# Performance work log

Measured on AMD Instinct MI355X. Metric: run time of the kernel, lower is better.

Reference implementation:

```python
import jax, jax.numpy as jnp
import numpy as np

MASS, CHARGE, ALPHA, BETA = 1.0, 0.5, 0.1, 0.05
ETA = jnp.array([1.0, -1.0, -1.0, -1.0], dtype=jnp.float32)  # Minkowski metric diag


def setup_inputs() -> dict:
    key = jax.random.key(0)
    k1, k2, k3 = jax.random.split(key, 3)
    B = 262144
    y = jax.random.normal(k1, (B, 8), dtype=jnp.float32)
    W = jax.random.normal(k2, (4, 4), dtype=jnp.float32) * 0.3
    V = jax.random.normal(k3, (4, 4), dtype=jnp.float32) * 0.3
    return {"y": y, "W": W, "V": V}


def _lagrangian(z):
    # z = (x, u, A) concatenated, shape [12]
    x, u, A = z[0:4], z[4:8], z[8:12]
    kinetic = 0.5 * MASS * jnp.sum(ETA * u * u)
    coupling = CHARGE * jnp.sum(ETA * u * A)
    xu_term = ALPHA * jnp.sum((x * u) ** 2)      # makes J_xu nontrivial
    uA_term = BETA * jnp.sum(u * A) ** 2          # makes J_Au nontrivial
    return kinetic + coupling + xu_term + uA_term


def reference(y, W, V):
    def A_vec(x):  # vector potential A^mu(x), works on [4] or [B,4]
        return jnp.tanh(x @ W.T) + x @ V.T

    x = y[:, 0:4]   # [B,4] positions
    u = y[:, 4:8]   # [B,4] velocities
    A = A_vec(x)    # [B,4]
    z = jnp.concatenate([x, u, A], axis=1)  # [B,12] = (x,u,A)

    gradL = jax.vmap(jax.grad(_lagrangian))(z)      # [B,12]
    H = jax.vmap(jax.hessian(_lagrangian))(z)       # [B,12,12]

    dL_dx = gradL[:, 0:4]
    dL_dA = gradL[:, 8:12]
    J_xu = H[:, 0:4, 4:8]    # d^2L/(dx^mu du^nu)
    J_uu = H[:, 4:8, 4:8]    # d^2L/(du^mu du^nu)
    J_Au = H[:, 8:12, 4:8]   # d^2L/(dA^mu du^nu)

    # dA_dx[a, nu, i] = dA^i/dx^nu (matches tf.stack(..., axis=2) layout)
    jacA = jax.vmap(jax.jacfwd(A_vec))(x)           # [B, i, nu]
    dA_dx = jnp.transpose(jacA, (0, 2, 1))          # [B, nu, i]

    J_uu_inv = jnp.linalg.pinv(J_uu)                # [B,4,4]

    force = (dL_dx
             + jnp.einsum('ajk,ak->aj', dA_dx, dL_dA)
             - jnp.einsum('ai,aij->aj', u,
                          J_xu + jnp.einsum('ajk,akm->ajm', dA_dx, J_Au)))
    acceleration = jnp.einsum('ai,aij->aj', force, J_uu_inv)  # [B,4]
    return acceleration
```

## Files before the change

kernel.cpp:

```cpp
#include <hip/hip_runtime.h>
#include <math.h>


__global__ __launch_bounds__(256) void rel_particle_kernel(
    const float* __restrict__ y, const float* __restrict__ W,
    const float* __restrict__ V, float* __restrict__ out, int B)
{
    __shared__ double sW[16], sV[16];
    if (threadIdx.x < 16)      sW[threadIdx.x]      = (double)W[threadIdx.x];
    else if (threadIdx.x < 32) sV[threadIdx.x - 16] = (double)V[threadIdx.x - 16];
    __syncthreads();

    int i = blockIdx.x * blockDim.x + threadIdx.x;
    if (i >= B) return;

    const float4* y4 = (const float4*)y;
    float4 xv = y4[2 * i];
    float4 uv = y4[2 * i + 1];
    double x[4] = {xv.x, xv.y, xv.z, xv.w};
    double u[4] = {uv.x, uv.y, uv.z, uv.w};
    const double eta[4] = {1.0, -1.0, -1.0, -1.0};
    const double CHG = 0.5, ALPHA = 0.1, BETA = 0.05;
    const double C2 = 2.0 * BETA;

    double A[4], G[4][4];
    #pragma unroll
    for (int j = 0; j < 4; ++j) {
        double t = 0.0, s = 0.0;
        #pragma unroll
        for (int k = 0; k < 4; ++k) {
            t += sW[j * 4 + k] * x[k];
            s += sV[j * 4 + k] * x[k];
        }
        double th = tanh(t);
        A[j] = th + s;
        double dth = 1.0 - th * th;
        #pragma unroll
        for (int k = 0; k < 4; ++k)
            G[j][k] = dth * sW[j * 4 + k] + sV[j * 4 + k];
    }

    double S = 0.0;
    #pragma unroll
    for (int k = 0; k < 4; ++k) S += u[k] * A[k];

    double P[4], R[4], Q[4];
    #pragma unroll
    for (int j = 0; j < 4; ++j) {
        double p = 0.0, r = 0.0, q = 0.0;
        #pragma unroll
        for (int k = 0; k < 4; ++k) {
            p += G[k][j] * u[k];
            r += G[j][k] * u[k];
            q += G[k][j] * (CHG * eta[k]) * u[k];
        }
        P[j] = p; R[j] = r; Q[j] = q;
    }
    double T = 0.0;
    #pragma unroll
    for (int j = 0; j < 4; ++j) T += u[j] * R[j];

    double f[4];
    #pragma unroll
    for (int j = 0; j < 4; ++j) {
        f[j] = -2.0 * ALPHA * x[j] * u[j] * u[j]
             + Q[j]
             + 2.0 * BETA * S * P[j]
             - (CHG * eta[j] + 2.0 * BETA * S) * R[j]
             - 2.0 * BETA * A[j] * T;
    }

    double d[4], mind = 1e300;
    #pragma unroll
    for (int j = 0; j < 4; ++j) {
        d[j] = eta[j] + 2.0 * ALPHA * x[j] * x[j];
        double a = fabs(d[j]);
        mind = (a < mind) ? a : mind;
    }

    double p01 = d[0] * d[1], p23 = d[2] * d[3];
    double det = p01 * p23;
    {
        double padj0 = d[1] * p23, padj1 = d[0] * p23;
        double padj2 = p01 * d[3], padj3 = p01 * d[2];
        det += C2 * (A[0]*A[0]*padj0 + A[1]*A[1]*padj1 +
                     A[2]*A[2]*padj2 + A[3]*A[3]*padj3);
    }

    double sumA2 = 0.0, sumA4 = 0.0, F2 = 0.0;
    #pragma unroll
    for (int j = 0; j < 4; ++j) {
        double Aj2 = A[j] * A[j];
        sumA2 += Aj2; sumA4 += Aj2 * Aj2;
        double Jjj = d[j] + C2 * Aj2;
        F2 += Jjj * Jjj;
    }
    F2 += C2 * C2 * (sumA2 * sumA2 - sumA4);
    double rowmax = 0.0;
    #pragma unroll
    for (int r = 0; r < 4; ++r) {
        double rs = 0.0;
        #pragma unroll
        for (int c = 0; c < 4; ++c) {
            double Jrc = C2 * A[r] * A[c] + ((r == c) ? d[r] : 0.0);
            rs += fabs(Jrc);
        }
        rowmax = (rs > rowmax) ? rs : rowmax;
    }
    double sig_hi2 = rowmax * rowmax;
    sig_hi2 = (F2 < sig_hi2) ? F2 : sig_hi2;
    bool safe = (fabs(det) > 2.8610229e-5 * sig_hi2 * sig_hi2) && (mind > 1e-3);

    double acc[4];
    if (safe) {
        double b[4], fd[4], den = 1.0, w = 0.0;
        #pragma unroll
        for (int j = 0; j < 4; ++j) {
            double inv = 1.0 / d[j];
            b[j]  = A[j] * inv;
            fd[j] = f[j] * inv;
            den  += C2 * A[j] * b[j];
            w    += b[j] * f[j];
        }
        double scale = C2 * w / den;
        #pragma unroll
        for (int j = 0; j < 4; ++j) acc[j] = fd[j] - b[j] * scale;
    } else {
        double M[4][4], Vm[4][4];
        #pragma unroll
        for (int r = 0; r < 4; ++r) {
            #pragma unroll
            for (int c2i = 0; c2i < 4; ++c2i) {
                M[r][c2i] = C2 * A[r] * A[c2i];
                Vm[r][c2i] = (r == c2i) ? 1.0 : 0.0;
            }
            M[r][r] += d[r];
        }
        for (int sweep = 0; sweep < 8; ++sweep) {
            #pragma unroll
            for (int p = 0; p < 3; ++p) {
                #pragma unroll
                for (int q2 = p + 1; q2 < 4; ++q2) {
                    double apq = M[p][q2];
                    if (fabs(apq) < 1e-280) continue;
                    double app = M[p][p], aqq = M[q2][q2];
                    double tau = (aqq - app) / (2.0 * apq);
                    double tt = ((tau >= 0.0) ? 1.0 : -1.0) /
                                (fabs(tau) + sqrt(1.0 + tau * tau));
                    double c = 1.0 / sqrt(1.0 + tt * tt);
                    double s = tt * c;
                    #pragma unroll
                    for (int k = 0; k < 4; ++k) {
                        double mkp = M[k][p], mkq = M[k][q2];
                        M[k][p]  = c * mkp - s * mkq;
                        M[k][q2] = s * mkp + c * mkq;
                    }
                    #pragma unroll
                    for (int k = 0; k < 4; ++k) {
                        double mpk = M[p][k], mqk = M[q2][k];
                        M[p][k]  = c * mpk - s * mqk;
                        M[q2][k] = s * mpk + c * mqk;
                    }
                    #pragma unroll
                    for (int k = 0; k < 4; ++k) {
                        double vkp = Vm[k][p], vkq = Vm[k][q2];
                        Vm[k][p]  = c * vkp - s * vkq;
                        Vm[k][q2] = s * vkp + c * vkq;
                    }
                }
            }
        }
        double lam[4], sigmax = 0.0;
        #pragma unroll
        for (int k = 0; k < 4; ++k) {
            lam[k] = M[k][k];
            double a = fabs(lam[k]);
            sigmax = (a > sigmax) ? a : sigmax;
        }
        double cutoff = 4.76837158203125e-6 * sigmax;
        #pragma unroll
        for (int j = 0; j < 4; ++j) acc[j] = 0.0;
        #pragma unroll
        for (int e = 0; e < 4; ++e) {
            if (fabs(lam[e]) > cutoff) {
                double coef = 0.0;
                #pragma unroll
                for (int k = 0; k < 4; ++k) coef += Vm[k][e] * f[k];
                coef /= lam[e];
                #pragma unroll
                for (int j = 0; j < 4; ++j) acc[j] += coef * Vm[j][e];
            }
        }
    }

    float4 res;
    res.x = (float)acc[0];
    res.y = (float)acc[1];
    res.z = (float)acc[2];
    res.w = (float)acc[3];
    ((float4*)out)[i] = res;
}

extern "C" void kernel_launch(void* const* d_in, const int* in_sizes, int n_in,
                              void* d_out, int out_size, void* d_ws, size_t ws_size,
                              hipStream_t stream) {
    const float* y = (const float*)d_in[0];
    const float* W = (const float*)d_in[1];
    const float* V = (const float*)d_in[2];
    float* out = (float*)d_out;
    int B = in_sizes[0] / 8;
    int block = 256;
    int grid = (B + block - 1) / block;
    rel_particle_kernel<<<grid, block, 0, stream>>>(y, W, V, out, B);
}
```

Before: 98.32 us.

## Split ill-conditioned particles into a compacted second pass for Jacobi solve

The fast kernel now handles only well-conditioned particles with the Sherman-Morrison solve. Particles that need the pseudo-inverse are appended to a workspace list through an atomic counter. A second small kernel recomputes the model terms for those listed particles and runs the Jacobi eigen-solve, which keeps the heavy branch out of the main kernel's register pressure and warp divergence. The cost is a memset, an extra launch, atomics, and recomputation for the flagged elements. If the workspace overflows, the remaining particles fall back to the Sherman-Morrison solve, which can be inaccurate.

```diff
diff --git a/kernel.cpp b/kernel.cpp
--- a/kernel.cpp
+++ b/kernel.cpp
@@ -2,9 +2,151 @@
 #include <math.h>
 
 
-__global__ __launch_bounds__(256) void rel_particle_kernel(
+#define SIX_RCOND 2.86102294921875e-5
+#define RCOND     4.76837158203125e-6
+
+__device__ __forceinline__ void model_terms(
+    const double* sW, const double* sV,
+    const double x[4], const double u[4],
+    double A[4], double f[4], double d[4])
+{
+    const double eta[4] = {1.0, -1.0, -1.0, -1.0};
+    const double CHG = 0.5, ALPHA = 0.1, BETA = 0.05;
+    double G[4][4];
+    #pragma unroll
+    for (int j = 0; j < 4; ++j) {
+        double t = 0.0, s = 0.0;
+        #pragma unroll
+        for (int k = 0; k < 4; ++k) { t += sW[j*4+k]*x[k]; s += sV[j*4+k]*x[k]; }
+        double th = tanh(t);
+        A[j] = th + s;
+        double dth = 1.0 - th * th;
+        #pragma unroll
+        for (int k = 0; k < 4; ++k) G[j][k] = dth * sW[j*4+k] + sV[j*4+k];
+    }
+    double S = 0.0;
+    #pragma unroll
+    for (int k = 0; k < 4; ++k) S += u[k] * A[k];
+    double P[4], R[4], Q[4];
+    #pragma unroll
+    for (int j = 0; j < 4; ++j) {
+        double p = 0.0, r = 0.0, q = 0.0;
+        #pragma unroll
+        for (int k = 0; k < 4; ++k) {
+            p += G[k][j] * u[k];
+            r += G[j][k] * u[k];
+            q += G[k][j] * (CHG * eta[k]) * u[k];
+        }
+        P[j] = p; R[j] = r; Q[j] = q;
+    }
+    double T = 0.0;
+    #pragma unroll
+    for (int j = 0; j < 4; ++j) T += u[j] * R[j];
+    #pragma unroll
+    for (int j = 0; j < 4; ++j) {
+        f[j] = -2.0 * ALPHA * x[j] * u[j] * u[j]
+             + Q[j]
+             + 2.0 * BETA * S * P[j]
+             - (CHG * eta[j] + 2.0 * BETA * S) * R[j]
+             - 2.0 * BETA * A[j] * T;
+        d[j] = eta[j] + 2.0 * ALPHA * x[j] * x[j];
+    }
+}
+
+__device__ __forceinline__ void sm_solve(
+    const double d[4], const double A[4], const double f[4], double acc[4])
+{
+    const double C2 = 0.1;
+    double b[4], fd[4], den = 1.0, w = 0.0;
+    #pragma unroll
+    for (int j = 0; j < 4; ++j) {
+        double inv = 1.0 / d[j];
+        b[j]  = A[j] * inv;
+        fd[j] = f[j] * inv;
+        den  += C2 * A[j] * b[j];
+        w    += b[j] * f[j];
+    }
+    double scale = C2 * w / den;
+    #pragma unroll
+    for (int j = 0; j < 4; ++j) acc[j] = fd[j] - b[j] * scale;
+}
+
+__device__ void jacobi_pinv_solve(
+    const double d[4], const double A[4], const double f[4], double acc[4])
+{
+    const double C2 = 0.1;
+    double M[4][4], Vm[4][4];
+    #pragma unroll
+    for (int r = 0; r < 4; ++r) {
+        #pragma unroll
+        for (int c = 0; c < 4; ++c) {
+            M[r][c] = C2 * A[r] * A[c];
+            Vm[r][c] = (r == c) ? 1.0 : 0.0;
+        }
+        M[r][r] += d[r];
+    }
+    for (int sweep = 0; sweep < 8; ++sweep) {
+        #pragma unroll
+        for (int p = 0; p < 3; ++p) {
+            #pragma unroll
+            for (int q2 = p + 1; q2 < 4; ++q2) {
+                double apq = M[p][q2];
+                if (fabs(apq) < 1e-280) continue;
+                double app = M[p][p], aqq = M[q2][q2];
+                double tau = (aqq - app) / (2.0 * apq);
+                double tt = ((tau >= 0.0) ? 1.0 : -1.0) /
+                            (fabs(tau) + sqrt(1.0 + tau * tau));
+                double c = 1.0 / sqrt(1.0 + tt * tt);
+                double s = tt * c;
+                #pragma unroll
+                for (int k = 0; k < 4; ++k) {
+                    double mkp = M[k][p], mkq = M[k][q2];
+                    M[k][p]  = c * mkp - s * mkq;
+                    M[k][q2] = s * mkp + c * mkq;
+                }
+                #pragma unroll
+                for (int k = 0; k < 4; ++k) {
+                    double mpk = M[p][k], mqk = M[q2][k];
+                    M[p][k]  = c * mpk - s * mqk;
+                    M[q2][k] = s * mpk + c * mqk;
+                }
+                #pragma unroll
+                for (int k = 0; k < 4; ++k) {
+                    double vkp = Vm[k][p], vkq = Vm[k][q2];
+                    Vm[k][p]  = c * vkp - s * vkq;
+                    Vm[k][q2] = s * vkp + c * vkq;
+                }
+            }
+        }
+    }
+    double lam[4], sigmax = 0.0;
+    #pragma unroll
+    for (int k = 0; k < 4; ++k) {
+        lam[k] = M[k][k];
+        double a = fabs(lam[k]);
+        sigmax = (a > sigmax) ? a : sigmax;
+    }
+    double cutoff = RCOND * sigmax;
+    #pragma unroll
+    for (int j = 0; j < 4; ++j) acc[j] = 0.0;
+    #pragma unroll
+    for (int e = 0; e < 4; ++e) {
+        if (fabs(lam[e]) > cutoff) {
+            double coef = 0.0;
+            #pragma unroll
+            for (int k = 0; k < 4; ++k) coef += Vm[k][e] * f[k];
+            coef /= lam[e];
+            #pragma unroll
+            for (int j = 0; j < 4; ++j) acc[j] += coef * Vm[j][e];
+        }
+    }
+}
+
+__global__ __launch_bounds__(256) void fast_kernel(
     const float* __restrict__ y, const float* __restrict__ W,
-    const float* __restrict__ V, float* __restrict__ out, int B)
+    const float* __restrict__ V, float* __restrict__ out,
+    unsigned int* __restrict__ cnt, int* __restrict__ list,
+    unsigned int cap, int B)
 {
     __shared__ double sW[16], sV[16];
     if (threadIdx.x < 16)      sW[threadIdx.x]      = (double)W[threadIdx.x];
@@ -19,74 +161,21 @@
     float4 uv = y4[2 * i + 1];
     double x[4] = {xv.x, xv.y, xv.z, xv.w};
     double u[4] = {uv.x, uv.y, uv.z, uv.w};
-    const double eta[4] = {1.0, -1.0, -1.0, -1.0};
-    const double CHG = 0.5, ALPHA = 0.1, BETA = 0.05;
-    const double C2 = 2.0 * BETA;
-
-    double A[4], G[4][4];
-    #pragma unroll
-    for (int j = 0; j < 4; ++j) {
-        double t = 0.0, s = 0.0;
-        #pragma unroll
-        for (int k = 0; k < 4; ++k) {
-            t += sW[j * 4 + k] * x[k];
-            s += sV[j * 4 + k] * x[k];
-        }
-        double th = tanh(t);
-        A[j] = th + s;
-        double dth = 1.0 - th * th;
-        #pragma unroll
-        for (int k = 0; k < 4; ++k)
-            G[j][k] = dth * sW[j * 4 + k] + sV[j * 4 + k];
-    }
-
-    double S = 0.0;
-    #pragma unroll
-    for (int k = 0; k < 4; ++k) S += u[k] * A[k];
-
-    double P[4], R[4], Q[4];
-    #pragma unroll
-    for (int j = 0; j < 4; ++j) {
-        double p = 0.0, r = 0.0, q = 0.0;
-        #pragma unroll
-        for (int k = 0; k < 4; ++k) {
-            p += G[k][j] * u[k];
-            r += G[j][k] * u[k];
-            q += G[k][j] * (CHG * eta[k]) * u[k];
-        }
-        P[j] = p; R[j] = r; Q[j] = q;
-    }
-    double T = 0.0;
-    #pragma unroll
-    for (int j = 0; j < 4; ++j) T += u[j] * R[j];
-
-    double f[4];
-    #pragma unroll
-    for (int j = 0; j < 4; ++j) {
-        f[j] = -2.0 * ALPHA * x[j] * u[j] * u[j]
-             + Q[j]
-             + 2.0 * BETA * S * P[j]
-             - (CHG * eta[j] + 2.0 * BETA * S) * R[j]
-             - 2.0 * BETA * A[j] * T;
-    }
-
-    double d[4], mind = 1e300;
-    #pragma unroll
-    for (int j = 0; j < 4; ++j) {
-        d[j] = eta[j] + 2.0 * ALPHA * x[j] * x[j];
+
+    double A[4], f[4], d[4];
+    model_terms(sW, sV, x, u, A, f, d);
+
+    const double C2 = 0.1;
+    double mind = 1e300;
+    #pragma unroll
+    for (int j = 0; j < 4; ++j) {
         double a = fabs(d[j]);
         mind = (a < mind) ? a : mind;
     }
-
     double p01 = d[0] * d[1], p23 = d[2] * d[3];
-    double det = p01 * p23;
-    {
-        double padj0 = d[1] * p23, padj1 = d[0] * p23;
-        double padj2 = p01 * d[3], padj3 = p01 * d[2];
-        det += C2 * (A[0]*A[0]*padj0 + A[1]*A[1]*padj1 +
-                     A[2]*A[2]*padj2 + A[3]*A[3]*padj3);
-    }
-
+    double det = p01 * p23
+        + C2 * (A[0]*A[0]*(d[1]*p23) + A[1]*A[1]*(d[0]*p23) +
+                A[2]*A[2]*(p01*d[3]) + A[3]*A[3]*(p01*d[2]));
     double sumA2 = 0.0, sumA4 = 0.0, F2 = 0.0;
     #pragma unroll
     for (int j = 0; j < 4; ++j) {
@@ -109,96 +198,60 @@
     }
     double sig_hi2 = rowmax * rowmax;
     sig_hi2 = (F2 < sig_hi2) ? F2 : sig_hi2;
-    bool safe = (fabs(det) > 2.8610229e-5 * sig_hi2 * sig_hi2) && (mind > 1e-3);
-
-    double acc[4];
+    bool safe = (fabs(det) > SIX_RCOND * sig_hi2 * sig_hi2) && (mind > 1e-3);
+
     if (safe) {
-        double b[4], fd[4], den = 1.0, w = 0.0;
-        #pragma unroll
-        for (int j = 0; j < 4; ++j) {
-            double inv = 1.0 / d[j];
-            b[j]  = A[j] * inv;
-            fd[j] = f[j] * inv;
-            den  += C2 * A[j] * b[j];
-            w    += b[j] * f[j];
-        }
-        double scale = C2 * w / den;
-        #pragma unroll
-        for (int j = 0; j < 4; ++j) acc[j] = fd[j] - b[j] * scale;
+        double acc[4];
+        sm_solve(d, A, f, acc);
+        float4 res;
+        res.x = (float)acc[0]; res.y = (float)acc[1];
+        res.z = (float)acc[2]; res.w = (float)acc[3];
+        ((float4*)out)[i] = res;
     } else {
-        double M[4][4], Vm[4][4];
-        #pragma unroll
-        for (int r = 0; r < 4; ++r) {
-            #pragma unroll
-            for (int c2i = 0; c2i < 4; ++c2i) {
-                M[r][c2i] = C2 * A[r] * A[c2i];
-                Vm[r][c2i] = (r == c2i) ? 1.0 : 0.0;
-            }
-            M[r][r] += d[r];
-        }
-        for (int sweep = 0; sweep < 8; ++sweep) {
-            #pragma unroll
-            for (int p = 0; p < 3; ++p) {
-                #pragma unroll
-                for (int q2 = p + 1; q2 < 4; ++q2) {
-                    double apq = M[p][q2];
-                    if (fabs(apq) < 1e-280) continue;
-                    double app = M[p][p], aqq = M[q2][q2];
-                    double tau = (aqq - app) / (2.0 * apq);
-                    double tt = ((tau >= 0.0) ? 1.0 : -1.0) /
-                                (fabs(tau) + sqrt(1.0 + tau * tau));
-                    double c = 1.0 / sqrt(1.0 + tt * tt);
-                    double s = tt * c;
-                    #pragma unroll
-                    for (int k = 0; k < 4; ++k) {
-                        double mkp = M[k][p], mkq = M[k][q2];
-                        M[k][p]  = c * mkp - s * mkq;
-                        M[k][q2] = s * mkp + c * mkq;
-                    }
-                    #pragma unroll
-                    for (int k = 0; k < 4; ++k) {
-                        double mpk = M[p][k], mqk = M[q2][k];
-                        M[p][k]  = c * mpk - s * mqk;
-                        M[q2][k] = s * mpk + c * mqk;
-                    }
-                    #pragma unroll
-                    for (int k = 0; k < 4; ++k) {
-                        double vkp = Vm[k][p], vkq = Vm[k][q2];
-                        Vm[k][p]  = c * vkp - s * vkq;
-                        Vm[k][q2] = s * vkp + c * vkq;
-                    }
-                }
-            }
-        }
-        double lam[4], sigmax = 0.0;
-        #pragma unroll
-        for (int k = 0; k < 4; ++k) {
-            lam[k] = M[k][k];
-            double a = fabs(lam[k]);
-            sigmax = (a > sigmax) ? a : sigmax;
-        }
-        double cutoff = 4.76837158203125e-6 * sigmax;
-        #pragma unroll
-        for (int j = 0; j < 4; ++j) acc[j] = 0.0;
-        #pragma unroll
-        for (int e = 0; e < 4; ++e) {
-            if (fabs(lam[e]) > cutoff) {
-                double coef = 0.0;
-                #pragma unroll
-                for (int k = 0; k < 4; ++k) coef += Vm[k][e] * f[k];
-                coef /= lam[e];
-                #pragma unroll
-                for (int j = 0; j < 4; ++j) acc[j] += coef * Vm[j][e];
-            }
-        }
-    }
-
-    float4 res;
-    res.x = (float)acc[0];
-    res.y = (float)acc[1];
-    res.z = (float)acc[2];
-    res.w = (float)acc[3];
-    ((float4*)out)[i] = res;
+        unsigned int idx = atomicAdd(cnt, 1u);
+        if (idx < cap) {
+            list[idx] = i;
+        } else {
+            double acc[4];
+            sm_solve(d, A, f, acc);
+            float4 res;
+            res.x = (float)acc[0]; res.y = (float)acc[1];
+            res.z = (float)acc[2]; res.w = (float)acc[3];
+            ((float4*)out)[i] = res;
+        }
+    }
+}
+
+__global__ __launch_bounds__(256) void slow_kernel(
+    const float* __restrict__ y, const float* __restrict__ W,
+    const float* __restrict__ V, float* __restrict__ out,
+    const unsigned int* __restrict__ cnt, const int* __restrict__ list,
+    unsigned int cap)
+{
+    __shared__ double sW[16], sV[16];
+    if (threadIdx.x < 16)      sW[threadIdx.x]      = (double)W[threadIdx.x];
+    else if (threadIdx.x < 32) sV[threadIdx.x - 16] = (double)V[threadIdx.x - 16];
+    __syncthreads();
+
+    unsigned int n = *cnt;
+    if (n > cap) n = cap;
+    int stride = gridDim.x * blockDim.x;
+    for (unsigned int j = blockIdx.x * blockDim.x + threadIdx.x; j < n; j += stride) {
+        int i = list[j];
+        const float4* y4 = (const float4*)y;
+        float4 xv = y4[2 * i];
+        float4 uv = y4[2 * i + 1];
+        double x[4] = {xv.x, xv.y, xv.z, xv.w};
+        double u[4] = {uv.x, uv.y, uv.z, uv.w};
+        double A[4], f[4], d[4];
+        model_terms(sW, sV, x, u, A, f, d);
+        double acc[4];
+        jacobi_pinv_solve(d, A, f, acc);
+        float4 res;
+        res.x = (float)acc[0]; res.y = (float)acc[1];
+        res.z = (float)acc[2]; res.w = (float)acc[3];
+        ((float4*)out)[i] = res;
+    }
 }
 
 extern "C" void kernel_launch(void* const* d_in, const int* in_sizes, int n_in,
@@ -209,7 +262,16 @@
     const float* V = (const float*)d_in[2];
     float* out = (float*)d_out;
     int B = in_sizes[0] / 8;
+
+    unsigned int* cnt = (unsigned int*)d_ws;
+    int* list = (int*)((char*)d_ws + 16);
+    unsigned int cap = (ws_size > 16) ? (unsigned int)((ws_size - 16) / sizeof(int)) : 0u;
+    if (cap > (unsigned int)B) cap = (unsigned int)B;
+
+    hipMemsetAsync(d_ws, 0, 16, stream);
+
     int block = 256;
     int grid = (B + block - 1) / block;
-    rel_particle_kernel<<<grid, block, 0, stream>>>(y, W, V, out, B);
-}
+    fast_kernel<<<grid, block, 0, stream>>>(y, W, V, out, cnt, list, cap, B);
+    slow_kernel<<<64, block, 0, stream>>>(y, W, V, out, cnt, list, cap);
+}
```

After: 88.36 us. -10.1%, faster.
